# Kernel optimization log

Hardware: AMD Instinct MI355X
Metric: run time of the kernel (lower is better)

## Reference

```python
import jax, jax.numpy as jnp
import numpy as np

N, D, H, K, L, C = 65536, 512, 256, 16, 3, 64  # n_support, embed_dim, D//2, max_clusters, num_levels, n_classes
EPS = 1e-5


def setup_inputs() -> dict:
    key = jax.random.key(0)
    ks = jax.random.split(key, 18)
    s = 0.02
    inp = {
        "support_features": jax.random.normal(ks[0], (N, D), jnp.float32),
        "support_labels": jax.random.randint(ks[1], (N,), 0, C),
        # cluster heads (per level): Linear(D,H) -> ReLU -> Linear(H,K) -> Softmax
        "ch_w1": jax.random.normal(ks[2], (L, D, H), jnp.float32) * s,
        "ch_b1": jnp.zeros((L, H), jnp.float32),
        "ch_w2": jax.random.normal(ks[3], (L, H, K), jnp.float32) * s,
        "ch_b2": jnp.zeros((L, K), jnp.float32),
        # prototype refiners (per level): Linear(D,D) -> LayerNorm -> ReLU -> Linear(D,D)
        "ref_w1": jax.random.normal(ks[4], (L, D, D), jnp.float32) * s,
        "ref_b1": jnp.zeros((L, D), jnp.float32),
        "ln_g": jnp.ones((L, D), jnp.float32),
        "ln_b": jnp.zeros((L, D), jnp.float32),
        "ref_w2": jax.random.normal(ks[5], (L, D, D), jnp.float32) * s,
        "ref_b2": jnp.zeros((L, D), jnp.float32),
        # hierarchy combiner: Linear(L*D, D) -> ReLU -> Linear(D, D)
        "comb_w1": jax.random.normal(ks[6], (L * D, D), jnp.float32) * s,
        "comb_b1": jnp.zeros((D,), jnp.float32),
        "comb_w2": jax.random.normal(ks[7], (D, D), jnp.float32) * s,
        "comb_b2": jnp.zeros((D,), jnp.float32),
    }
    return inp


def _layernorm(x, g, b):
    m = x.mean(-1, keepdims=True)
    v = ((x - m) ** 2).mean(-1, keepdims=True)
    return (x - m) * jax.lax.rsqrt(v + EPS) * g + b


def reference(support_features, support_labels, ch_w1, ch_b1, ch_w2, ch_b2,
              ref_w1, ref_b1, ln_g, ln_b, ref_w2, ref_b2,
              comb_w1, comb_b1, comb_w2, comb_b2):
    current = support_features  # [N, D]; per-class offsets applied via label gather
    level_protos = []
    for l in range(L):
        # cluster head; softmax omitted since argmax is softmax-invariant
        logits = jax.nn.relu(current @ ch_w1[l] + ch_b1[l]) @ ch_w2[l] + ch_b2[l]  # [N, K]
        assign = jnp.argmax(logits, axis=-1)  # [N]
        seg = support_labels * K + assign  # combined (class, cluster) segment id
        sums = jax.ops.segment_sum(current, seg, num_segments=C * K)  # [C*K, D]
        cnt = jax.ops.segment_sum(jnp.ones((N,), current.dtype), seg, num_segments=C * K)
        means = sums / jnp.maximum(cnt, 1.0)[:, None]  # empty clusters -> 0, masked below
        h = means @ ref_w1[l] + ref_b1[l]
        h = jax.nn.relu(_layernorm(h, ln_g[l], ln_b[l]))
        refined = (h @ ref_w2[l] + ref_b2[l]).reshape(C, K, D)
        ne = (cnt.reshape(C, K) > 0).astype(current.dtype)  # non-empty cluster mask
        lp = (refined * ne[..., None]).sum(1) / ne.sum(1)[:, None]  # [C, D] mean over non-empty
        level_protos.append(lp)
        current = current + lp[support_labels]
    combined = jnp.concatenate(level_protos, axis=-1)  # [C, L*D]
    protos = jax.nn.relu(combined @ comb_w1 + comb_b1) @ comb_w2 + comb_b2  # [C, D]
    return protos
```

## Files before the change

### kernel.cpp

```cpp
#include <hip/hip_runtime.h>

#define NPTS 65536
#define DIM  512
#define HID  256
#define KCL  16
#define NLVL 3
#define NCLS 64
#define NSEG (NCLS*KCL)
#define EPSF 1e-5f

typedef __bf16 bf16_t;
typedef bf16_t bf16x4 __attribute__((ext_vector_type(4)));
typedef bf16_t bf16x8 __attribute__((ext_vector_type(8)));
typedef float  f32x4  __attribute__((ext_vector_type(4)));

#define LDA 40
#define LDH 132

__global__ __launch_bounds__(256) void wsplit_kernel(
    const float* __restrict__ w1, bf16_t* __restrict__ hiT, bf16_t* __restrict__ loT)
{
  int gid = blockIdx.x * 256 + threadIdx.x;
  int n = gid >> 9, k = gid & 511;
  int l = n >> 8, j = n & 255;
  float v = w1[l*DIM*HID + k*HID + j];
  bf16_t h = (bf16_t)v;
  hiT[gid] = h;
  loT[gid] = (bf16_t)(v - (float)h);
}

__global__ __launch_bounds__(256) void wsplit2_kernel(
    const float* __restrict__ w1, const float* __restrict__ w2,
    bf16_t* __restrict__ h1, bf16_t* __restrict__ l1,
    bf16_t* __restrict__ h2, bf16_t* __restrict__ l2)
{
  const int per = NLVL*DIM*DIM;
  int gid = blockIdx.x * 256 + threadIdx.x;
  const float* w = (gid < per) ? w1 : w2;
  bf16_t* hh = (gid < per) ? h1 : h2;
  bf16_t* ll = (gid < per) ? l1 : l2;
  int g2 = (gid < per) ? gid : gid - per;
  int n512 = g2 >> 9, k = g2 & 511;
  int l = n512 >> 9, n = n512 & 511;
  float v = w[(size_t)l*DIM*DIM + (size_t)k*DIM + n];
  bf16_t h = (bf16_t)v;
  hh[g2] = h;
  ll[g2] = (bf16_t)(v - (float)h);
}

__global__ __launch_bounds__(256) void wsplitW2_kernel(
    const float* __restrict__ w2, bf16_t* __restrict__ hiT, bf16_t* __restrict__ loT)
{
  int gid = blockIdx.x * 256 + threadIdx.x;
  int l = gid >> 12, rem = gid & 4095;
  int k2 = rem >> 8, k = rem & 255;
  float v = w2[(size_t)l*HID*KCL + k*KCL + k2];
  bf16_t h = (bf16_t)v;
  hiT[gid] = h;
  loT[gid] = (bf16_t)(v - (float)h);
}

__global__ __launch_bounds__(256, 2) void gemmassign_kernel(
    const float* __restrict__ feat,
    const bf16_t* __restrict__ BhiT, const bf16_t* __restrict__ BloT,
    const bf16_t* __restrict__ w2hT, const bf16_t* __restrict__ w2lT,
    const float* __restrict__ offsrc, int ldo,
    const int* __restrict__ labels,
    const float* __restrict__ pb2,
    int* __restrict__ asg, int* __restrict__ cnt)
{
  __shared__ __align__(16) unsigned char SMraw[640*LDA*2];
  __shared__ int labs[64];
  bf16_t* SM  = (bf16_t*)SMraw;
  bf16_t* Ahi = SM;
  bf16_t* Alo = SM + 64*LDA;
  bf16_t* Bhi = SM + 128*LDA;
  bf16_t* Blo = SM + 384*LDA;

  const int t = threadIdx.x;
  const int row0 = blockIdx.x * 64;
  const int w = t >> 6, lane = t & 63;
  const int fm = lane & 15, fq = lane >> 4;

  if (t < 64) labs[t] = labels[row0 + t];
  const float pv = pb2[fm];

  f32x4 acc[4][4];
  #pragma unroll
  for (int i = 0; i < 4; i++)
    #pragma unroll
    for (int j = 0; j < 4; j++)
      #pragma unroll
      for (int r = 0; r < 4; r++) acc[i][j][r] = 0.f;

  for (int kc = 0; kc < DIM; kc += 32) {
    __syncthreads();
    #pragma unroll
    for (int p = 0; p < 2; p++) {
      int idx = t + 256*p;
      int r = idx >> 3, c = idx & 7;
      float4 v = *(const float4*)&feat[(size_t)(row0 + r)*DIM + kc + c*4];
      bf16x4 hi, lo;
      hi[0] = (bf16_t)v.x; lo[0] = (bf16_t)(v.x - (float)hi[0]);
      hi[1] = (bf16_t)v.y; lo[1] = (bf16_t)(v.y - (float)hi[1]);
      hi[2] = (bf16_t)v.z; lo[2] = (bf16_t)(v.z - (float)hi[2]);
      hi[3] = (bf16_t)v.w; lo[3] = (bf16_t)(v.w - (float)hi[3]);
      *(bf16x4*)&Ahi[r*LDA + c*4] = hi;
      *(bf16x4*)&Alo[r*LDA + c*4] = lo;
    }
    #pragma unroll
    for (int p = 0; p < 4; p++) {
      int idx = t + 256*p;
      int n = idx >> 2, c = idx & 3;
      *(bf16x8*)&Bhi[n*LDA + c*8] = *(const bf16x8*)&BhiT[(size_t)n*DIM + kc + c*8];
      *(bf16x8*)&Blo[n*LDA + c*8] = *(const bf16x8*)&BloT[(size_t)n*DIM + kc + c*8];
    }
    __syncthreads();

    bf16x8 ah[4], al[4], bh[4], bl[4];
    #pragma unroll
    for (int mt = 0; mt < 4; mt++) {
      int rr = (mt*16 + fm)*LDA + fq*8;
      ah[mt] = *(bf16x8*)&Ahi[rr];
      al[mt] = *(bf16x8*)&Alo[rr];
    }
    #pragma unroll
    for (int nt = 0; nt < 4; nt++) {
      int rr = (w*64 + nt*16 + fm)*LDA + fq*8;
      bh[nt] = *(bf16x8*)&Bhi[rr];
      bl[nt] = *(bf16x8*)&Blo[rr];
    }
    #pragma unroll
    for (int mt = 0; mt < 4; mt++)
      #pragma unroll
      for (int nt = 0; nt < 4; nt++) {
        acc[mt][nt] = __builtin_amdgcn_mfma_f32_16x16x32_bf16(ah[mt], bh[nt], acc[mt][nt], 0, 0, 0);
        acc[mt][nt] = __builtin_amdgcn_mfma_f32_16x16x32_bf16(ah[mt], bl[nt], acc[mt][nt], 0, 0, 0);
        acc[mt][nt] = __builtin_amdgcn_mfma_f32_16x16x32_bf16(al[mt], bh[nt], acc[mt][nt], 0, 0, 0);
      }
  }

  __syncthreads();
  float* hS = (float*)SMraw;

  f32x4 lg = {0.f, 0.f, 0.f, 0.f};

  #pragma unroll
  for (int p = 0; p < 2; p++) {
    #pragma unroll
    for (int c2 = 0; c2 < 2; c2++) {
      int nt = 2*p + c2;
      int col = w*64 + nt*16 + fm;
      int kk  = w*32 + c2*16 + fm;
      #pragma unroll
      for (int mt = 0; mt < 4; mt++)
        #pragma unroll
        for (int r = 0; r < 4; r++) {
          int row = mt*16 + fq*4 + r;
          float hv = fmaxf(acc[mt][nt][r] + offsrc[(size_t)labs[row]*ldo + col], 0.f);
          hS[row*LDH + kk] = hv;
        }
    }
    __syncthreads();

    #pragma unroll
    for (int s = 0; s < 4; s++) {
      f32x4 a0 = *(f32x4*)&hS[(w*16 + fm)*LDH + s*32 + fq*8];
      f32x4 a1 = *(f32x4*)&hS[(w*16 + fm)*LDH + s*32 + fq*8 + 4];
      bf16x8 ahf, alf;
      #pragma unroll
      for (int j = 0; j < 4; j++) {
        bf16_t h0 = (bf16_t)a0[j]; ahf[j]   = h0; alf[j]   = (bf16_t)(a0[j] - (float)h0);
        bf16_t h1 = (bf16_t)a1[j]; ahf[4+j] = h1; alf[4+j] = (bf16_t)(a1[j] - (float)h1);
      }
      int kb = s*64 + p*32 + fq*8;
      bf16x8 bhf = *(const bf16x8*)&w2hT[fm*HID + kb];
      bf16x8 blf = *(const bf16x8*)&w2lT[fm*HID + kb];
      lg = __builtin_amdgcn_mfma_f32_16x16x32_bf16(ahf, bhf, lg, 0, 0, 0);
      lg = __builtin_amdgcn_mfma_f32_16x16x32_bf16(ahf, blf, lg, 0, 0, 0);
      lg = __builtin_amdgcn_mfma_f32_16x16x32_bf16(alf, bhf, lg, 0, 0, 0);
    }
    if (p == 0) __syncthreads();
  }

  #pragma unroll
  for (int r = 0; r < 4; r++) {
    float v = lg[r] + pv;
    int idx = fm;
    #pragma unroll
    for (int ofs = 8; ofs > 0; ofs >>= 1) {
      float ov = __shfl_xor(v, ofs, 16);
      int   oi = __shfl_xor(idx, ofs, 16);
      if (ov > v || (ov == v && oi < idx)) { v = ov; idx = oi; }
    }
    if (fm == 0) {
      int rloc = w*16 + fq*4 + r;
      asg[row0 + rloc] = idx;
      atomicAdd(&cnt[labs[rloc]*KCL + idx], 1);
    }
  }
}

__global__ __launch_bounds__(256) void gemm64_kernel(
    const float* __restrict__ Asrc,
    const bf16_t* __restrict__ BhiT, const bf16_t* __restrict__ BloT,
    float* __restrict__ C, int mode,
    const int* __restrict__ cnt, const float* __restrict__ off,
    const float* __restrict__ b1, const float* __restrict__ g,
    const float* __restrict__ bb,
    const float* __restrict__ mS, const float* __restrict__ rS)
{
  __shared__ __align__(16) bf16_t Ahi[64*LDA];
  __shared__ __align__(16) bf16_t Alo[64*LDA];
  __shared__ __align__(16) bf16_t Bhi[64*LDA];
  __shared__ __align__(16) bf16_t Blo[64*LDA];
  __shared__ float rm[64], rr_[64];

  const int t = threadIdx.x;
  const int row0 = blockIdx.x * 64, col0 = blockIdx.y * 64;
  const int w = t >> 6, lane = t & 63;
  const int wm = w & 1, wn = w >> 1;
  const int fm = lane & 15, fq = lane >> 4;

  if (t < 64) {
    if (mode == 1) {
      int n = cnt[row0 + t];
      rm[t] = (float)n;
      rr_[t] = 1.f / fmaxf((float)n, 1.f);
    } else {
      rm[t] = mS[row0 + t];
      rr_[t] = rS[row0 + t];
    }
  }

  f32x4 acc[2][2];
  #pragma unroll
  for (int i = 0; i < 2; i++)
    #pragma unroll
    for (int j = 0; j < 2; j++)
      #pragma unroll
      for (int r = 0; r < 4; r++) acc[i][j][r] = 0.f;

  for (int kc = 0; kc < DIM; kc += 32) {
    __syncthreads();
    #pragma unroll
    for (int p = 0; p < 2; p++) {
      int idx = t + 256*p;
      int r = idx >> 3, c = idx & 7;
      float4 v = *(const float4*)&Asrc[(size_t)(row0 + r)*DIM + kc + c*4];
      if (mode == 1) {
        int cls = (row0 + r) >> 4;
        float4 o = *(const float4*)&off[(size_t)cls*DIM + kc + c*4];
        float n = rm[r], inv = rr_[r];
        v.x = (v.x + n*o.x) * inv; v.y = (v.y + n*o.y) * inv;
        v.z = (v.z + n*o.z) * inv; v.w = (v.w + n*o.w) * inv;
      } else {
        float4 B1 = *(const float4*)&b1[kc + c*4];
        float4 G4 = *(const float4*)&g[kc + c*4];
        float4 BB = *(const float4*)&bb[kc + c*4];
        float m = rm[r], rs = rr_[r];
        v.x = fmaxf((v.x + B1.x - m)*rs*G4.x + BB.x, 0.f);
        v.y = fmaxf((v.y + B1.y - m)*rs*G4.y + BB.y, 0.f);
        v.z = fmaxf((v.z + B1.z - m)*rs*G4.z + BB.z, 0.f);
        v.w = fmaxf((v.w + B1.w - m)*rs*G4.w + BB.w, 0.f);
      }
      bf16x4 hi, lo;
      hi[0] = (bf16_t)v.x; lo[0] = (bf16_t)(v.x - (float)hi[0]);
      hi[1] = (bf16_t)v.y; lo[1] = (bf16_t)(v.y - (float)hi[1]);
      hi[2] = (bf16_t)v.z; lo[2] = (bf16_t)(v.z - (float)hi[2]);
      hi[3] = (bf16_t)v.w; lo[3] = (bf16_t)(v.w - (float)hi[3]);
      *(bf16x4*)&Ahi[r*LDA + c*4] = hi;
      *(bf16x4*)&Alo[r*LDA + c*4] = lo;
    }
    {
      int n = t >> 2, kof = (t & 3)*8;
      *(bf16x8*)&Bhi[n*LDA + kof] = *(const bf16x8*)&BhiT[(size_t)(col0 + n)*DIM + kc + kof];
      *(bf16x8*)&Blo[n*LDA + kof] = *(const bf16x8*)&BloT[(size_t)(col0 + n)*DIM + kc + kof];
    }
    __syncthreads();

    bf16x8 ah[2], al[2], bh[2], bl[2];
    #pragma unroll
    for (int mt = 0; mt < 2; mt++) {
      int idx = (wm*32 + mt*16 + fm)*LDA + fq*8;
      ah[mt] = *(bf16x8*)&Ahi[idx];
      al[mt] = *(bf16x8*)&Alo[idx];
    }
    #pragma unroll
    for (int nt = 0; nt < 2; nt++) {
      int idx = (wn*32 + nt*16 + fm)*LDA + fq*8;
      bh[nt] = *(bf16x8*)&Bhi[idx];
      bl[nt] = *(bf16x8*)&Blo[idx];
    }
    #pragma unroll
    for (int mt = 0; mt < 2; mt++)
      #pragma unroll
      for (int nt = 0; nt < 2; nt++) {
        acc[mt][nt] = __builtin_amdgcn_mfma_f32_16x16x32_bf16(ah[mt], bh[nt], acc[mt][nt], 0, 0, 0);
        acc[mt][nt] = __builtin_amdgcn_mfma_f32_16x16x32_bf16(ah[mt], bl[nt], acc[mt][nt], 0, 0, 0);
        acc[mt][nt] = __builtin_amdgcn_mfma_f32_16x16x32_bf16(al[mt], bh[nt], acc[mt][nt], 0, 0, 0);
        acc[mt][nt] = __builtin_amdgcn_mfma_f32_16x16x32_bf16(al[mt], bl[nt], acc[mt][nt], 0, 0, 0);
      }
  }

  #pragma unroll
  for (int mt = 0; mt < 2; mt++)
    #pragma unroll
    for (int nt = 0; nt < 2; nt++) {
      int col = col0 + wn*32 + nt*16 + fm;
      int rowb = row0 + wm*32 + mt*16 + fq*4;
      #pragma unroll
      for (int r = 0; r < 4; r++)
        C[(size_t)(rowb + r)*DIM + col] = acc[mt][nt][r];
    }
}

__global__ __launch_bounds__(256) void lnstats_kernel(
    const float* __restrict__ Y1, const float* __restrict__ b1,
    float* __restrict__ mS, float* __restrict__ rS)
{
  int r = blockIdx.x, t = threadIdx.x;
  float x0 = Y1[(size_t)r*DIM + t]       + b1[t];
  float x1 = Y1[(size_t)r*DIM + t + 256] + b1[t + 256];
  float s1 = x0 + x1, s2 = x0*x0 + x1*x1;
  #pragma unroll
  for (int ofs = 32; ofs > 0; ofs >>= 1) {
    s1 += __shfl_xor(s1, ofs);
    s2 += __shfl_xor(s2, ofs);
  }
  __shared__ float r1[4], r2[4];
  int lane = t & 63, w = t >> 6;
  if (lane == 0) { r1[w] = s1; r2[w] = s2; }
  __syncthreads();
  if (t == 0) {
    s1 = r1[0] + r1[1] + r1[2] + r1[3];
    s2 = r2[0] + r2[1] + r2[2] + r2[3];
    float m = s1 * (1.f/512.f);
    float var = s2 * (1.f/512.f) - m*m;
    mS[r] = m;
    rS[r] = rsqrtf(var + EPSF);
  }
}

__global__ __launch_bounds__(256) void protoOffgemm_kernel(
    const float* __restrict__ Y2, const float* __restrict__ b2,
    const int* __restrict__ cnt, float* __restrict__ off, float* __restrict__ lp_out,
    const float* __restrict__ w1next, const float* __restrict__ b1next,
    float* __restrict__ offW1b)
{
  __shared__ float offs[DIM];
  int c = blockIdx.x, t = threadIdx.x;
  int nes = 0;
  #pragma unroll
  for (int k = 0; k < KCL; k++) nes += (cnt[c*KCL + k] > 0);
  float inv = 1.f / (float)nes;
  #pragma unroll
  for (int h = 0; h < 2; h++) {
    int d = t + h*256;
    float s = 0.f;
    #pragma unroll
    for (int k = 0; k < KCL; k++)
      if (cnt[c*KCL + k] > 0) s += Y2[(size_t)(c*KCL + k)*DIM + d];
    float lp = s * inv + b2[d];
    lp_out[c*DIM + d] = lp;
    float on = off[c*DIM + d] + lp;
    off[c*DIM + d] = on;
    offs[d] = on;
  }
  if (w1next == nullptr) return;
  __syncthreads();
  float a = 0.f;
  #pragma unroll 4
  for (int d = 0; d < DIM; d++)
    a = fmaf(offs[d], w1next[d*HID + t], a);
  offW1b[c*HID + t] = a + b1next[t];
}

__global__ void scan_kernel(const int* __restrict__ cnt, int* __restrict__ seg_st,
                            int* __restrict__ cursor)
{
  int t = threadIdx.x;
  int4 v = *(const int4*)&cnt[t*4];
  int a0 = v.x, a1 = v.x + v.y, a2 = a1 + v.z, tot = a2 + v.w;
  int lane = t & 63, w = t >> 6;
  int sc = tot;
  #pragma unroll
  for (int ofs = 1; ofs < 64; ofs <<= 1) {
    int u = __shfl_up(sc, ofs);
    if (lane >= ofs) sc += u;
  }
  __shared__ int wt[4];
  if (lane == 63) wt[w] = sc;
  __syncthreads();
  int base = 0;
  #pragma unroll
  for (int i = 0; i < 4; i++) if (i < w) base += wt[i];
  int excl = base + sc - tot;
  seg_st[t*4 + 1] = excl + a0;
  seg_st[t*4 + 2] = excl + a1;
  seg_st[t*4 + 3] = excl + a2;
  seg_st[t*4 + 4] = excl + tot;
  if (t == 0) seg_st[0] = 0;
  int4 cur = {excl, excl + a0, excl + a1, excl + a2};
  *(int4*)&cursor[t*4] = cur;
}

__global__ __launch_bounds__(256) void scatter_kernel(
    const int* __restrict__ labels, const int* __restrict__ asg,
    int* __restrict__ cursor, int* __restrict__ rowlist, int* __restrict__ seglist)
{
  int i = blockIdx.x * 256 + threadIdx.x;
  int seg = labels[i]*KCL + asg[i];
  int pos = atomicAdd(&cursor[seg], 1);
  rowlist[pos] = i;
  seglist[pos] = seg;
}

__global__ __launch_bounds__(256) void means3_kernel(
    const float* __restrict__ feat, const int* __restrict__ rowlist,
    const int* __restrict__ seglist, float* __restrict__ sums)
{
  __shared__ int rows[64];
  __shared__ int segs[65];
  int t = threadIdx.x;
  int i0 = blockIdx.x * 64;
  int col = blockIdx.y * 256 + t;
  if (t < 64) { rows[t] = rowlist[i0 + t]; segs[t] = seglist[i0 + t]; }
  if (t == 64) segs[64] = -1;
  __syncthreads();
  float acc = 0.f;
  for (int base = 0; base < 64; base += 16) {
    float v[16];
    #pragma unroll
    for (int j = 0; j < 16; j++)
      v[j] = feat[(size_t)rows[base + j]*DIM + col];
    #pragma unroll
    for (int j = 0; j < 16; j++) {
      acc += v[j];
      if (segs[base + j] != segs[base + j + 1]) {
        atomicAdd(&sums[(size_t)segs[base + j]*DIM + col], acc);
        acc = 0.f;
      }
    }
  }
}

__global__ __launch_bounds__(256) void fgemm1_kernel(
    const float* __restrict__ lp_all, const float* __restrict__ cw1,
    float* __restrict__ Hacc)
{
  __shared__ float As[64*132];
  __shared__ float Ws[128*64];
  int t = threadIdx.x;
  int nc = blockIdx.x * 64, kc = blockIdx.y * 128;

  #pragma unroll
  for (int p = 0; p < 8; p++) {
    int i = t + 256*p;
    int m = i >> 5, k0 = (i & 31) << 2;
    int k = kc + k0;
    int l = k >> 9, d = k & 511;
    *(float4*)&As[m*132 + k0] = *(const float4*)&lp_all[(size_t)(l*NCLS + m)*DIM + d];
  }
  #pragma unroll
  for (int p = 0; p < 8; p++) {
    int i = t + 256*p;
    int k = i >> 4, n0 = (i & 15) << 2;
    *(float4*)&Ws[k*64 + n0] = *(const float4*)&cw1[(size_t)(kc + k)*DIM + nc + n0];
  }
  __syncthreads();

  int tn = (t & 15) * 4, tmg = (t >> 4) * 4;
  float acc[4][4];
  #pragma unroll
  for (int i = 0; i < 4; i++)
    #pragma unroll
    for (int j = 0; j < 4; j++) acc[i][j] = 0.f;

  for (int k = 0; k < 128; k += 4) {
    float4 a[4], w[4];
    #pragma unroll
    for (int i = 0; i < 4; i++) a[i] = *(float4*)&As[(tmg + i)*132 + k];
    #pragma unroll
    for (int j = 0; j < 4; j++) w[j] = *(float4*)&Ws[(k + j)*64 + tn];
    #pragma unroll
    for (int kk = 0; kk < 4; kk++) {
      float wv[4] = {w[kk].x, w[kk].y, w[kk].z, w[kk].w};
      float av[4] = {a[0][kk], a[1][kk], a[2][kk], a[3][kk]};
      #pragma unroll
      for (int i = 0; i < 4; i++)
        #pragma unroll
        for (int j = 0; j < 4; j++)
          acc[i][j] = fmaf(av[i], wv[j], acc[i][j]);
    }
  }
  #pragma unroll
  for (int i = 0; i < 4; i++)
    #pragma unroll
    for (int j = 0; j < 4; j++)
      atomicAdd(&Hacc[(size_t)(tmg + i)*DIM + nc + tn + j], acc[i][j]);
}

__global__ __launch_bounds__(256) void fgemm2_kernel(
    const float* __restrict__ Hacc, const float* __restrict__ cb1,
    const float* __restrict__ cw2, float* __restrict__ Oacc)
{
  __shared__ float As[64*132];
  __shared__ float Ws[128*64];
  int t = threadIdx.x;
  int nc = blockIdx.x * 64, kc = blockIdx.y * 128;

  #pragma unroll
  for (int p = 0; p < 8; p++) {
    int i = t + 256*p;
    int m = i >> 5, k0 = (i & 31) << 2;
    float4 v = *(const float4*)&Hacc[(size_t)m*DIM + kc + k0];
    float4 b = *(const float4*)&cb1[kc + k0];
    v.x = fmaxf(v.x + b.x, 0.f); v.y = fmaxf(v.y + b.y, 0.f);
    v.z = fmaxf(v.z + b.z, 0.f); v.w = fmaxf(v.w + b.w, 0.f);
    *(float4*)&As[m*132 + k0] = v;
  }
  #pragma unroll
  for (int p = 0; p < 8; p++) {
    int i = t + 256*p;
    int k = i >> 4, n0 = (i & 15) << 2;
    *(float4*)&Ws[k*64 + n0] = *(const float4*)&cw2[(size_t)(kc + k)*DIM + nc + n0];
  }
  __syncthreads();

  int tn = (t & 15) * 4, tmg = (t >> 4) * 4;
  float acc[4][4];
  #pragma unroll
  for (int i = 0; i < 4; i++)
    #pragma unroll
    for (int j = 0; j < 4; j++) acc[i][j] = 0.f;

  for (int k = 0; k < 128; k += 4) {
    float4 a[4], w[4];
    #pragma unroll
    for (int i = 0; i < 4; i++) a[i] = *(float4*)&As[(tmg + i)*132 + k];
    #pragma unroll
    for (int j = 0; j < 4; j++) w[j] = *(float4*)&Ws[(k + j)*64 + tn];
    #pragma unroll
    for (int kk = 0; kk < 4; kk++) {
      float wv[4] = {w[kk].x, w[kk].y, w[kk].z, w[kk].w};
      float av[4] = {a[0][kk], a[1][kk], a[2][kk], a[3][kk]};
      #pragma unroll
      for (int i = 0; i < 4; i++)
        #pragma unroll
        for (int j = 0; j < 4; j++)
          acc[i][j] = fmaf(av[i], wv[j], acc[i][j]);
    }
  }
  #pragma unroll
  for (int i = 0; i < 4; i++)
    #pragma unroll
    for (int j = 0; j < 4; j++)
      atomicAdd(&Oacc[(size_t)(tmg + i)*DIM + nc + tn + j], acc[i][j]);
}

__global__ __launch_bounds__(256) void fbias_kernel(
    const float* __restrict__ Oacc, const float* __restrict__ cb2,
    float* __restrict__ out)
{
  int gi = blockIdx.x * 256 + threadIdx.x;
  out[gi] = Oacc[gi] + cb2[gi & 511];
}

extern "C" void kernel_launch(void* const* d_in, const int* in_sizes, int n_in,
                              void* d_out, int out_size, void* d_ws, size_t ws_size,
                              hipStream_t stream) {
  const float* feat   = (const float*)d_in[0];
  const int*   labels = (const int*)d_in[1];
  const float* ch_w1  = (const float*)d_in[2];
  const float* ch_b1  = (const float*)d_in[3];
  const float* ch_w2  = (const float*)d_in[4];
  const float* ch_b2  = (const float*)d_in[5];
  const float* ref_w1 = (const float*)d_in[6];
  const float* ref_b1 = (const float*)d_in[7];
  const float* ln_g   = (const float*)d_in[8];
  const float* ln_b   = (const float*)d_in[9];
  const float* ref_w2 = (const float*)d_in[10];
  const float* ref_b2 = (const float*)d_in[11];
  const float* cw1    = (const float*)d_in[12];
  const float* cb1    = (const float*)d_in[13];
  const float* cw2    = (const float*)d_in[14];
  const float* cb2    = (const float*)d_in[15];
  float* out = (float*)d_out;

  float* wsf = (float*)d_ws;
  float* off    = wsf;
  float* lp_all = off + 32768;
  float* sums   = lp_all + 98304;
  int*   cnt_i  = (int*)(sums + 524288);
  float* offW1b = sums + 524288 + 1024;
  float* Hacc   = offW1b + 16384;
  float* Oacc   = Hacc + 32768;
  float* Y1     = Oacc + 32768;
  float* Y2     = Y1 + 524288;
  float* mS     = Y2 + 524288;
  float* rS     = mS + 1024;

  bf16_t* whiT  = (bf16_t*)(rS + 1024);
  bf16_t* wloT  = whiT + (size_t)NLVL*HID*DIM;
  bf16_t* r1hiT = wloT + (size_t)NLVL*HID*DIM;
  bf16_t* r1loT = r1hiT + (size_t)NLVL*DIM*DIM;
  bf16_t* r2hiT = r1loT + (size_t)NLVL*DIM*DIM;
  bf16_t* r2loT = r2hiT + (size_t)NLVL*DIM*DIM;
  int* asg     = (int*)(r2loT + (size_t)NLVL*DIM*DIM);
  int* rowlist = asg + NPTS;
  int* seglist = rowlist + NPTS;
  int* seg_st  = seglist + NPTS;
  int* cursor  = seg_st + 1040;
  bf16_t* w2hT = (bf16_t*)(cursor + NSEG);
  bf16_t* w2lT = w2hT + (size_t)NLVL*KCL*HID;

  hipMemsetAsync(off, 0, NCLS*DIM*sizeof(float), stream);

  wsplit_kernel<<<NLVL*HID*DIM/256, 256, 0, stream>>>(ch_w1, whiT, wloT);
  wsplit2_kernel<<<2*NLVL*DIM*DIM/256, 256, 0, stream>>>(
      ref_w1, ref_w2, r1hiT, r1loT, r2hiT, r2loT);
  wsplitW2_kernel<<<NLVL*KCL*HID/256, 256, 0, stream>>>(ch_w2, w2hT, w2lT);

  for (int l = 0; l < NLVL; l++) {
    hipMemsetAsync(sums, 0, (NSEG*DIM + NSEG)*sizeof(float), stream);

    const float* offsrc = (l == 0) ? ch_b1 : offW1b;
    int ldo = (l == 0) ? 0 : HID;

    gemmassign_kernel<<<NPTS/64, 256, 0, stream>>>(
        feat, whiT + (size_t)l*HID*DIM, wloT + (size_t)l*HID*DIM,
        w2hT + (size_t)l*KCL*HID, w2lT + (size_t)l*KCL*HID,
        offsrc, ldo, labels,
        ch_b2 + (size_t)l*KCL,
        asg, cnt_i);

    scan_kernel<<<1, 256, 0, stream>>>(cnt_i, seg_st, cursor);

    scatter_kernel<<<NPTS/256, 256, 0, stream>>>(labels, asg, cursor, rowlist, seglist);

    means3_kernel<<<dim3(NPTS/64, DIM/256), 256, 0, stream>>>(
        feat, rowlist, seglist, sums);

    gemm64_kernel<<<dim3(NSEG/64, DIM/64), 256, 0, stream>>>(
        sums, r1hiT + (size_t)l*DIM*DIM, r1loT + (size_t)l*DIM*DIM, Y1, 1,
        cnt_i, off, nullptr, nullptr, nullptr, nullptr, nullptr);

    lnstats_kernel<<<NSEG, 256, 0, stream>>>(
        Y1, ref_b1 + (size_t)l*DIM, mS, rS);

    gemm64_kernel<<<dim3(NSEG/64, DIM/64), 256, 0, stream>>>(
        Y1, r2hiT + (size_t)l*DIM*DIM, r2loT + (size_t)l*DIM*DIM, Y2, 2,
        nullptr, nullptr, ref_b1 + (size_t)l*DIM,
        ln_g + (size_t)l*DIM, ln_b + (size_t)l*DIM, mS, rS);

    protoOffgemm_kernel<<<NCLS, 256, 0, stream>>>(
        Y2, ref_b2 + (size_t)l*DIM, cnt_i, off, lp_all + (size_t)l*NCLS*DIM,
        (l < NLVL-1) ? (ch_w1 + (size_t)(l+1)*DIM*HID) : nullptr,
        (l < NLVL-1) ? (ch_b1 + (size_t)(l+1)*HID) : nullptr,
        offW1b);
  }

  hipMemsetAsync(Hacc, 0, 2*NCLS*DIM*sizeof(float), stream);
  fgemm1_kernel<<<dim3(DIM/64, NLVL*DIM/128), 256, 0, stream>>>(lp_all, cw1, Hacc);
  fgemm2_kernel<<<dim3(DIM/64, DIM/128), 256, 0, stream>>>(Hacc, cb1, cw2, Oacc);
  fbias_kernel<<<NCLS*DIM/256, 256, 0, stream>>>(Oacc, cb2, out);
}
```

Baseline: 814.9 us.

## Split fused cluster-head GEMM+assign into 128x128 tiled GEMM and separate assign kernel

Replaces the fused kernel, which computed a 64-row by 256-col hidden tile and then ran the second layer and argmax in-block, with two kernels. The first is a square 128x128 tiled split-bf16 GEMM that writes the raw hidden pre-activations to a global buffer. The second reads them back, adds bias or offset, applies ReLU, runs the H->K MFMA and does the argmax. This gives better operand reuse per tile and more blocks, but adds a 64 MB write and read of the intermediate per level plus an extra launch.

Result: slower. 896.9 us (+10.1%).

```diff
diff --git a/kernel.cpp b/kernel.cpp
--- a/kernel.cpp
+++ b/kernel.cpp
@@ -15,7 +15,6 @@
 typedef float  f32x4  __attribute__((ext_vector_type(4)));
 
 #define LDA 40
-#define LDH 132
 
 __global__ __launch_bounds__(256) void wsplit_kernel(
     const float* __restrict__ w1, bf16_t* __restrict__ hiT, bf16_t* __restrict__ loT)
@@ -60,30 +59,21 @@
   loT[gid] = (bf16_t)(v - (float)h);
 }
 
-__global__ __launch_bounds__(256, 2) void gemmassign_kernel(
+__global__ __launch_bounds__(256, 2) void gemm128_kernel(
     const float* __restrict__ feat,
     const bf16_t* __restrict__ BhiT, const bf16_t* __restrict__ BloT,
-    const bf16_t* __restrict__ w2hT, const bf16_t* __restrict__ w2lT,
-    const float* __restrict__ offsrc, int ldo,
-    const int* __restrict__ labels,
-    const float* __restrict__ pb2,
-    int* __restrict__ asg, int* __restrict__ cnt)
-{
-  __shared__ __align__(16) unsigned char SMraw[640*LDA*2];
-  __shared__ int labs[64];
-  bf16_t* SM  = (bf16_t*)SMraw;
-  bf16_t* Ahi = SM;
-  bf16_t* Alo = SM + 64*LDA;
-  bf16_t* Bhi = SM + 128*LDA;
-  bf16_t* Blo = SM + 384*LDA;
+    float* __restrict__ G, int ldg)
+{
+  __shared__ __align__(16) bf16_t Ahi[128*LDA];
+  __shared__ __align__(16) bf16_t Alo[128*LDA];
+  __shared__ __align__(16) bf16_t Bhi[128*LDA];
+  __shared__ __align__(16) bf16_t Blo[128*LDA];
 
   const int t = threadIdx.x;
-  const int row0 = blockIdx.x * 64;
+  const int row0 = blockIdx.x * 128, col0 = blockIdx.y * 128;
   const int w = t >> 6, lane = t & 63;
+  const int wm = w & 1, wn = w >> 1;
   const int fm = lane & 15, fq = lane >> 4;
-
-  if (t < 64) labs[t] = labels[row0 + t];
-  const float pv = pb2[fm];
 
   f32x4 acc[4][4];
   #pragma unroll
@@ -96,7 +86,7 @@
   for (int kc = 0; kc < DIM; kc += 32) {
     __syncthreads();
     #pragma unroll
-    for (int p = 0; p < 2; p++) {
+    for (int p = 0; p < 4; p++) {
       int idx = t + 256*p;
       int r = idx >> 3, c = idx & 7;
       float4 v = *(const float4*)&feat[(size_t)(row0 + r)*DIM + kc + c*4];
@@ -109,24 +99,24 @@
       *(bf16x4*)&Alo[r*LDA + c*4] = lo;
     }
     #pragma unroll
-    for (int p = 0; p < 4; p++) {
+    for (int p = 0; p < 2; p++) {
       int idx = t + 256*p;
       int n = idx >> 2, c = idx & 3;
-      *(bf16x8*)&Bhi[n*LDA + c*8] = *(const bf16x8*)&BhiT[(size_t)n*DIM + kc + c*8];
-      *(bf16x8*)&Blo[n*LDA + c*8] = *(const bf16x8*)&BloT[(size_t)n*DIM + kc + c*8];
+      *(bf16x8*)&Bhi[n*LDA + c*8] = *(const bf16x8*)&BhiT[(size_t)(col0 + n)*DIM + kc + c*8];
+      *(bf16x8*)&Blo[n*LDA + c*8] = *(const bf16x8*)&BloT[(size_t)(col0 + n)*DIM + kc + c*8];
     }
     __syncthreads();
 
     bf16x8 ah[4], al[4], bh[4], bl[4];
     #pragma unroll
     for (int mt = 0; mt < 4; mt++) {
-      int rr = (mt*16 + fm)*LDA + fq*8;
+      int rr = (wm*64 + mt*16 + fm)*LDA + fq*8;
       ah[mt] = *(bf16x8*)&Ahi[rr];
       al[mt] = *(bf16x8*)&Alo[rr];
     }
     #pragma unroll
     for (int nt = 0; nt < 4; nt++) {
-      int rr = (w*64 + nt*16 + fm)*LDA + fq*8;
+      int rr = (wn*64 + nt*16 + fm)*LDA + fq*8;
       bh[nt] = *(bf16x8*)&Bhi[rr];
       bl[nt] = *(bf16x8*)&Blo[rr];
     }
@@ -140,47 +130,61 @@
       }
   }
 
+  #pragma unroll
+  for (int mt = 0; mt < 4; mt++)
+    #pragma unroll
+    for (int nt = 0; nt < 4; nt++) {
+      int col = col0 + wn*64 + nt*16 + fm;
+      int rowb = row0 + wm*64 + mt*16 + fq*4;
+      #pragma unroll
+      for (int r = 0; r < 4; r++)
+        G[(size_t)(rowb + r)*ldg + col] = acc[mt][nt][r];
+    }
+}
+
+__global__ __launch_bounds__(256) void assign3_kernel(
+    const float* __restrict__ Gl,
+    const bf16_t* __restrict__ w2hT, const bf16_t* __restrict__ w2lT,
+    const float* __restrict__ offsrc, int ldo,
+    const int* __restrict__ labels,
+    const float* __restrict__ pb2,
+    int* __restrict__ asg, int* __restrict__ cnt)
+{
+  __shared__ int labs[64];
+  const int t = threadIdx.x;
+  const int w = t >> 6, lane = t & 63;
+  const int fm = lane & 15, fq = lane >> 4;
+  const int row0 = blockIdx.x * 64;
+  if (t < 64) labs[t] = labels[row0 + t];
   __syncthreads();
-  float* hS = (float*)SMraw;
+
+  const int row = w*16 + fm;
+  const int lab = labs[row];
+  const float pv = pb2[fm];
+  const float* grow = &Gl[(size_t)(row0 + row)*HID];
+  const float* orow = &offsrc[(size_t)lab*ldo];
 
   f32x4 lg = {0.f, 0.f, 0.f, 0.f};
-
-  #pragma unroll
-  for (int p = 0; p < 2; p++) {
-    #pragma unroll
-    for (int c2 = 0; c2 < 2; c2++) {
-      int nt = 2*p + c2;
-      int col = w*64 + nt*16 + fm;
-      int kk  = w*32 + c2*16 + fm;
-      #pragma unroll
-      for (int mt = 0; mt < 4; mt++)
-        #pragma unroll
-        for (int r = 0; r < 4; r++) {
-          int row = mt*16 + fq*4 + r;
-          float hv = fmaxf(acc[mt][nt][r] + offsrc[(size_t)labs[row]*ldo + col], 0.f);
-          hS[row*LDH + kk] = hv;
-        }
-    }
-    __syncthreads();
-
-    #pragma unroll
-    for (int s = 0; s < 4; s++) {
-      f32x4 a0 = *(f32x4*)&hS[(w*16 + fm)*LDH + s*32 + fq*8];
-      f32x4 a1 = *(f32x4*)&hS[(w*16 + fm)*LDH + s*32 + fq*8 + 4];
-      bf16x8 ahf, alf;
-      #pragma unroll
-      for (int j = 0; j < 4; j++) {
-        bf16_t h0 = (bf16_t)a0[j]; ahf[j]   = h0; alf[j]   = (bf16_t)(a0[j] - (float)h0);
-        bf16_t h1 = (bf16_t)a1[j]; ahf[4+j] = h1; alf[4+j] = (bf16_t)(a1[j] - (float)h1);
-      }
-      int kb = s*64 + p*32 + fq*8;
-      bf16x8 bhf = *(const bf16x8*)&w2hT[fm*HID + kb];
-      bf16x8 blf = *(const bf16x8*)&w2lT[fm*HID + kb];
-      lg = __builtin_amdgcn_mfma_f32_16x16x32_bf16(ahf, bhf, lg, 0, 0, 0);
-      lg = __builtin_amdgcn_mfma_f32_16x16x32_bf16(ahf, blf, lg, 0, 0, 0);
-      lg = __builtin_amdgcn_mfma_f32_16x16x32_bf16(alf, bhf, lg, 0, 0, 0);
-    }
-    if (p == 0) __syncthreads();
+  #pragma unroll
+  for (int k0 = 0; k0 < HID; k0 += 32) {
+    int kb = k0 + fq*8;
+    f32x4 g0 = *(const f32x4*)&grow[kb];
+    f32x4 g1 = *(const f32x4*)&grow[kb + 4];
+    f32x4 o0 = *(const f32x4*)&orow[kb];
+    f32x4 o1 = *(const f32x4*)&orow[kb + 4];
+    bf16x8 ah, al;
+    #pragma unroll
+    for (int j = 0; j < 4; j++) {
+      float h0 = fmaxf(g0[j] + o0[j], 0.f);
+      float h1 = fmaxf(g1[j] + o1[j], 0.f);
+      bf16_t c0 = (bf16_t)h0; ah[j]   = c0; al[j]   = (bf16_t)(h0 - (float)c0);
+      bf16_t c1 = (bf16_t)h1; ah[4+j] = c1; al[4+j] = (bf16_t)(h1 - (float)c1);
+    }
+    bf16x8 bh = *(const bf16x8*)&w2hT[fm*HID + kb];
+    bf16x8 bl = *(const bf16x8*)&w2lT[fm*HID + kb];
+    lg = __builtin_amdgcn_mfma_f32_16x16x32_bf16(ah, bh, lg, 0, 0, 0);
+    lg = __builtin_amdgcn_mfma_f32_16x16x32_bf16(ah, bl, lg, 0, 0, 0);
+    lg = __builtin_amdgcn_mfma_f32_16x16x32_bf16(al, bh, lg, 0, 0, 0);
   }
 
   #pragma unroll
@@ -600,8 +604,9 @@
   float* Y2     = Y1 + 524288;
   float* mS     = Y2 + 524288;
   float* rS     = mS + 1024;
-
-  bf16_t* whiT  = (bf16_t*)(rS + 1024);
+  float* Gt     = rS + 1024;
+
+  bf16_t* whiT  = (bf16_t*)(Gt + (size_t)NPTS*HID);
   bf16_t* wloT  = whiT + (size_t)NLVL*HID*DIM;
   bf16_t* r1hiT = wloT + (size_t)NLVL*HID*DIM;
   bf16_t* r1loT = r1hiT + (size_t)NLVL*DIM*DIM;
@@ -625,15 +630,15 @@
   for (int l = 0; l < NLVL; l++) {
     hipMemsetAsync(sums, 0, (NSEG*DIM + NSEG)*sizeof(float), stream);
 
+    gemm128_kernel<<<dim3(NPTS/128, HID/128), 256, 0, stream>>>(
+        feat, whiT + (size_t)l*HID*DIM, wloT + (size_t)l*HID*DIM, Gt, HID);
+
     const float* offsrc = (l == 0) ? ch_b1 : offW1b;
     int ldo = (l == 0) ? 0 : HID;
 
-    gemmassign_kernel<<<NPTS/64, 256, 0, stream>>>(
-        feat, whiT + (size_t)l*HID*DIM, wloT + (size_t)l*HID*DIM,
-        w2hT + (size_t)l*KCL*HID, w2lT + (size_t)l*KCL*HID,
-        offsrc, ldo, labels,
-        ch_b2 + (size_t)l*KCL,
-        asg, cnt_i);
+    assign3_kernel<<<NPTS/64, 256, 0, stream>>>(
+        Gt, w2hT + (size_t)l*KCL*HID, w2lT + (size_t)l*KCL*HID,
+        offsrc, ldo, labels, ch_b2 + (size_t)l*KCL, asg, cnt_i);
 
     scan_kernel<<<1, 256, 0, stream>>>(cnt_i, seg_st, cursor);
 
```

## Enlarge gemmassign tile to 128 rows with 8-wave 2x4 layout

Applied to the files above, without the earlier changes.

The cluster-head GEMM block now covers 128 rows with 512 threads arranged as a 2x4 wave grid, instead of 64 rows with 4 waves. Each staged B tile (the W1 hi/lo split) is therefore reused across twice as many rows, which cuts global and LDS traffic for weights per row. The ReLU/second-layer epilogue is reorganised into four 64-column passes through a smaller shared buffer. The launch bound of (512, 4) caps registers tightly against a 64-float accumulator plus fragment registers, which risks spills. LDS use per block also rises, which limits how many blocks fit on a CU.

Measured after the change: 838.3 us. +2.9%, slower.

```diff
diff --git a/kernel.cpp b/kernel.cpp
--- a/kernel.cpp
+++ b/kernel.cpp
@@ -15,7 +15,7 @@
 typedef float  f32x4  __attribute__((ext_vector_type(4)));
 
 #define LDA 40
-#define LDH 132
+#define LDH2 68
 
 __global__ __launch_bounds__(256) void wsplit_kernel(
     const float* __restrict__ w1, bf16_t* __restrict__ hiT, bf16_t* __restrict__ loT)
@@ -60,7 +60,7 @@
   loT[gid] = (bf16_t)(v - (float)h);
 }
 
-__global__ __launch_bounds__(256, 2) void gemmassign_kernel(
+__global__ __launch_bounds__(512, 4) void gemmassign_kernel(
     const float* __restrict__ feat,
     const bf16_t* __restrict__ BhiT, const bf16_t* __restrict__ BloT,
     const bf16_t* __restrict__ w2hT, const bf16_t* __restrict__ w2lT,
@@ -69,20 +69,21 @@
     const float* __restrict__ pb2,
     int* __restrict__ asg, int* __restrict__ cnt)
 {
-  __shared__ __align__(16) unsigned char SMraw[640*LDA*2];
-  __shared__ int labs[64];
+  __shared__ __align__(16) unsigned char SMraw[768*LDA*2];
+  __shared__ int labs[128];
   bf16_t* SM  = (bf16_t*)SMraw;
   bf16_t* Ahi = SM;
-  bf16_t* Alo = SM + 64*LDA;
-  bf16_t* Bhi = SM + 128*LDA;
-  bf16_t* Blo = SM + 384*LDA;
+  bf16_t* Alo = SM + 128*LDA;
+  bf16_t* Bhi = SM + 256*LDA;
+  bf16_t* Blo = SM + 512*LDA;
 
   const int t = threadIdx.x;
-  const int row0 = blockIdx.x * 64;
+  const int row0 = blockIdx.x * 128;
   const int w = t >> 6, lane = t & 63;
+  const int wm = w & 1, wn = w >> 1;
   const int fm = lane & 15, fq = lane >> 4;
 
-  if (t < 64) labs[t] = labels[row0 + t];
+  if (t < 128) labs[t] = labels[row0 + t];
   const float pv = pb2[fm];
 
   f32x4 acc[4][4];
@@ -97,7 +98,7 @@
     __syncthreads();
     #pragma unroll
     for (int p = 0; p < 2; p++) {
-      int idx = t + 256*p;
+      int idx = t + 512*p;
       int r = idx >> 3, c = idx & 7;
       float4 v = *(const float4*)&feat[(size_t)(row0 + r)*DIM + kc + c*4];
       bf16x4 hi, lo;
@@ -109,8 +110,8 @@
       *(bf16x4*)&Alo[r*LDA + c*4] = lo;
     }
     #pragma unroll
-    for (int p = 0; p < 4; p++) {
-      int idx = t + 256*p;
+    for (int p = 0; p < 2; p++) {
+      int idx = t + 512*p;
       int n = idx >> 2, c = idx & 3;
       *(bf16x8*)&Bhi[n*LDA + c*8] = *(const bf16x8*)&BhiT[(size_t)n*DIM + kc + c*8];
       *(bf16x8*)&Blo[n*LDA + c*8] = *(const bf16x8*)&BloT[(size_t)n*DIM + kc + c*8];
@@ -120,13 +121,13 @@
     bf16x8 ah[4], al[4], bh[4], bl[4];
     #pragma unroll
     for (int mt = 0; mt < 4; mt++) {
-      int rr = (mt*16 + fm)*LDA + fq*8;
+      int rr = (wm*64 + mt*16 + fm)*LDA + fq*8;
       ah[mt] = *(bf16x8*)&Ahi[rr];
       al[mt] = *(bf16x8*)&Alo[rr];
     }
     #pragma unroll
     for (int nt = 0; nt < 4; nt++) {
-      int rr = (w*64 + nt*16 + fm)*LDA + fq*8;
+      int rr = (wn*64 + nt*16 + fm)*LDA + fq*8;
       bh[nt] = *(bf16x8*)&Bhi[rr];
       bl[nt] = *(bf16x8*)&Blo[rr];
     }
@@ -146,41 +147,43 @@
   f32x4 lg = {0.f, 0.f, 0.f, 0.f};
 
   #pragma unroll
-  for (int p = 0; p < 2; p++) {
-    #pragma unroll
-    for (int c2 = 0; c2 < 2; c2++) {
-      int nt = 2*p + c2;
-      int col = w*64 + nt*16 + fm;
-      int kk  = w*32 + c2*16 + fm;
-      #pragma unroll
-      for (int mt = 0; mt < 4; mt++)
+  for (int q = 0; q < 4; q++) {
+    if (wn == q) {
+      #pragma unroll
+      for (int nt = 0; nt < 4; nt++) {
+        int colq = nt*16 + fm;
+        int colg = q*64 + colq;
         #pragma unroll
-        for (int r = 0; r < 4; r++) {
-          int row = mt*16 + fq*4 + r;
-          float hv = fmaxf(acc[mt][nt][r] + offsrc[(size_t)labs[row]*ldo + col], 0.f);
-          hS[row*LDH + kk] = hv;
-        }
+        for (int mt = 0; mt < 4; mt++)
+          #pragma unroll
+          for (int r = 0; r < 4; r++) {
+            int row = wm*64 + mt*16 + fq*4 + r;
+            float hv = fmaxf(acc[mt][nt][r] +
+                             offsrc[(size_t)labs[row]*ldo + colg], 0.f);
+            hS[row*LDH2 + colq] = hv;
+          }
+      }
     }
     __syncthreads();
 
     #pragma unroll
-    for (int s = 0; s < 4; s++) {
-      f32x4 a0 = *(f32x4*)&hS[(w*16 + fm)*LDH + s*32 + fq*8];
-      f32x4 a1 = *(f32x4*)&hS[(w*16 + fm)*LDH + s*32 + fq*8 + 4];
+    for (int s = 0; s < 2; s++) {
+      int kb = s*32 + fq*8;
+      f32x4 a0 = *(f32x4*)&hS[(w*16 + fm)*LDH2 + kb];
+      f32x4 a1 = *(f32x4*)&hS[(w*16 + fm)*LDH2 + kb + 4];
       bf16x8 ahf, alf;
       #pragma unroll
       for (int j = 0; j < 4; j++) {
         bf16_t h0 = (bf16_t)a0[j]; ahf[j]   = h0; alf[j]   = (bf16_t)(a0[j] - (float)h0);
         bf16_t h1 = (bf16_t)a1[j]; ahf[4+j] = h1; alf[4+j] = (bf16_t)(a1[j] - (float)h1);
       }
-      int kb = s*64 + p*32 + fq*8;
-      bf16x8 bhf = *(const bf16x8*)&w2hT[fm*HID + kb];
-      bf16x8 blf = *(const bf16x8*)&w2lT[fm*HID + kb];
+      bf16x8 bhf = *(const bf16x8*)&w2hT[fm*HID + q*64 + kb];
+      bf16x8 blf = *(const bf16x8*)&w2lT[fm*HID + q*64 + kb];
       lg = __builtin_amdgcn_mfma_f32_16x16x32_bf16(ahf, bhf, lg, 0, 0, 0);
       lg = __builtin_amdgcn_mfma_f32_16x16x32_bf16(ahf, blf, lg, 0, 0, 0);
       lg = __builtin_amdgcn_mfma_f32_16x16x32_bf16(alf, bhf, lg, 0, 0, 0);
     }
-    if (p == 0) __syncthreads();
+    __syncthreads();
   }
 
   #pragma unroll
@@ -628,7 +631,7 @@
     const float* offsrc = (l == 0) ? ch_b1 : offW1b;
     int ldo = (l == 0) ? 0 : HID;
 
-    gemmassign_kernel<<<NPTS/64, 256, 0, stream>>>(
+    gemmassign_kernel<<<NPTS/128, 512, 0, stream>>>(
         feat, whiT + (size_t)l*HID*DIM, wloT + (size_t)l*HID*DIM,
         w2hT + (size_t)l*KCL*HID, w2lT + (size_t)l*KCL*HID,
         offsrc, ldo, labels,
```
